# Kernel optimization log

Measured on AMD Instinct MI355X. Metric: run time of the kernel, lower is better.

## Reference

```python
import jax, jax.numpy as jnp
import numpy as np

B, N, H, DH = 2, 512, 12, 64
DIM, DPAIR, DCOND = 768, 128, 512
INNER = 4 * DIM  # expansion_factor * dim


def _ln(x, eps=1e-5):
    m = jnp.mean(x, -1, keepdims=True)
    v = jnp.mean((x - m) ** 2, -1, keepdims=True)
    return (x - m) * jax.lax.rsqrt(v + eps)


def _rope(t):
    # t: [b,h,n,d]; standard rotary over head dim
    d = t.shape[-1]
    pos = jnp.arange(t.shape[2], dtype=t.dtype)
    inv = 1.0 / (10000.0 ** (jnp.arange(0, d, 2, dtype=t.dtype) / d))
    ang = pos[:, None] * inv[None, :]  # [n, d/2]
    cos, sin = jnp.cos(ang), jnp.sin(ang)
    t1, t2 = t[..., 0::2], t[..., 1::2]
    return jnp.stack([t1 * cos - t2 * sin, t1 * sin + t2 * cos], -1).reshape(t.shape)


def _adaln(x, cond, mask, gw, gb, bw):
    cn = _ln(cond)
    return (_ln(x) * jax.nn.sigmoid(cn @ gw + gb) + cn @ bw) * mask[..., None]


def _scale_out(x, cond, mask, w, b):
    # adaLN-zero style output scaling
    return x * jax.nn.sigmoid(_ln(cond) @ w + b) * mask[..., None]


def _windowed_attn(q, k, v, bias, pair_mask, n_queries, n_keys):
    # q/k/v: [b,h,n,d]; bias: [b,h,n,n]; pair_mask: [b,n,n]
    b, h, n, d = q.shape
    nw = n // n_queries
    centers = jnp.arange(nw) * n_queries + n_queries // 2
    idx = centers[:, None] - n_keys // 2 + jnp.arange(n_keys)[None, :]  # [nw,nk]
    valid = (idx >= 0) & (idx < n)
    idxc = jnp.clip(idx, 0, n - 1)
    qw = q.reshape(b, h, nw, n_queries, d)
    kw = k[:, :, idxc]  # [b,h,nw,nk,d]
    vw = v[:, :, idxc]
    ib = jnp.broadcast_to(idxc[None, None, :, None, :], (b, h, nw, n_queries, n_keys))
    bias_w = jnp.take_along_axis(bias.reshape(b, h, nw, n_queries, n), ib, axis=-1)
    pm = jnp.take_along_axis(
        pair_mask.reshape(b, nw, n_queries, n),
        jnp.broadcast_to(idxc[None, :, None, :], (b, nw, n_queries, n_keys)), axis=-1)
    scores = jnp.einsum('bhwqd,bhwkd->bhwqk', qw, kw) / jnp.sqrt(jnp.asarray(d, q.dtype)) + bias_w
    ok = (pm[:, None] > 0) & valid[None, None, :, None, :]
    attn = jax.nn.softmax(jnp.where(ok, scores, -1e9), axis=-1)
    out = jnp.einsum('bhwqk,bhwkd->bhwqd', attn, vw)
    return out.reshape(b, h, n, d)


def setup_inputs() -> dict:
    key = jax.random.key(0)
    ks = iter(jax.random.split(key, 48))
    nrm = lambda shape: jax.random.normal(next(ks), shape, jnp.float32) * 0.02
    return dict(
        x=jax.random.normal(next(ks), (B, N, DIM), jnp.float32),
        pair_rep=jax.random.normal(next(ks), (B, N, N, DPAIR), jnp.float32),
        cond=jax.random.normal(next(ks), (B, N, DCOND), jnp.float32),
        mask=jnp.ones((B, N), jnp.float32),
        pair_mask=jnp.ones((B, N, N), jnp.float32),
        adaln1_gw=nrm((DCOND, DIM)), adaln1_gb=jnp.zeros((DIM,), jnp.float32), adaln1_bw=nrm((DCOND, DIM)),
        wq=nrm((DIM, H * DH)), bq=jnp.zeros((H * DH,), jnp.float32),
        wk=nrm((DIM, H * DH)), bk=jnp.zeros((H * DH,), jnp.float32),
        wv=nrm((DIM, H * DH)), bv=jnp.zeros((H * DH,), jnp.float32),
        wg=nrm((DIM, H * DH)), bg=jnp.zeros((H * DH,), jnp.float32),
        wb_pair=nrm((DPAIR, H)),
        wo=nrm((H * DH, DIM)), bo=jnp.zeros((DIM,), jnp.float32),
        scale1_w=nrm((DCOND, DIM)), scale1_b=jnp.full((DIM,), -2.0, jnp.float32),
        adaln2_gw=nrm((DCOND, DIM)), adaln2_gb=jnp.zeros((DIM,), jnp.float32), adaln2_bw=nrm((DCOND, DIM)),
        tr_win=nrm((DIM, 2 * INNER)), tr_wout=nrm((INNER, DIM)),
        scale2_w=nrm((DCOND, DIM)), scale2_b=jnp.full((DIM,), -2.0, jnp.float32),
        n_queries=32, n_keys=128,
    )


def reference(x, pair_rep, cond, mask, pair_mask,
              adaln1_gw, adaln1_gb, adaln1_bw,
              wq, bq, wk, bk, wv, bv, wg, bg, wb_pair, wo, bo,
              scale1_w, scale1_b,
              adaln2_gw, adaln2_gb, adaln2_bw,
              tr_win, tr_wout,
              scale2_w, scale2_b,
              n_queries, n_keys):
    b, n, _ = x.shape
    x = x * mask[..., None]

    # --- MHA (adaLN -> pair-biased rotary windowed attention -> adaLN-zero scale) ---
    xa = _adaln(x, cond, mask, adaln1_gw, adaln1_gb, adaln1_bw)
    q = (xa @ wq + bq).reshape(b, n, H, DH).transpose(0, 2, 1, 3)
    k = (xa @ wk + bk).reshape(b, n, H, DH).transpose(0, 2, 1, 3)
    v = (xa @ wv + bv).reshape(b, n, H, DH).transpose(0, 2, 1, 3)
    q, k = _ln(q), _ln(k)      # qk layernorm
    q, k = _rope(q), _rope(k)  # rotary
    bias = jnp.einsum('bijp,ph->bhij', _ln(pair_rep), wb_pair)
    o = _windowed_attn(q, k, v, bias, pair_mask, n_queries, n_keys)
    o = o.transpose(0, 2, 1, 3).reshape(b, n, H * DH)
    attn_out = (o * jax.nn.sigmoid(xa @ wg + bg)) @ wo + bo
    attn_out = _scale_out(attn_out, cond, mask, scale1_w, scale1_b) * mask[..., None]
    x = (attn_out + x) * mask[..., None]  # residual_mha

    # --- Transition (adaLN -> SwiGLU -> adaLN-zero scale) ---
    xt = _adaln(x, cond, mask, adaln2_gw, adaln2_gb, adaln2_bw)
    a, g = jnp.split(xt @ tr_win, 2, axis=-1)
    tr = ((a * jax.nn.silu(g)) @ tr_wout) * mask[..., None]
    tr = _scale_out(tr, cond, mask, scale2_w, scale2_b) * mask[..., None]
    x = (tr + x) * mask[..., None]  # residual_transition
    return x * mask[..., None]
```

## Files before the change

### kernel.cpp

```cpp
#include <hip/hip_runtime.h>
#include <hip/hip_bf16.h>
#include <math.h>
#include <stdint.h>

#define Bc   2
#define Nc   512
#define Hc   12
#define DHc  64
#define DIMc 768
#define DPAIRc 128
#define DCONDc 512
#define INNERc 3072
#define NQc  32
#define NKc  128
#define NWc  (Nc / NQc)

typedef __attribute__((ext_vector_type(8))) short short8;
typedef __attribute__((ext_vector_type(4))) float floatx4;

__device__ inline float wave_sum(float v) {
#pragma unroll
  for (int off = 32; off > 0; off >>= 1) v += __shfl_xor(v, off, 64);
  return v;
}
__device__ inline float wave_max(float v) {
#pragma unroll
  for (int off = 32; off > 0; off >>= 1) v = fmaxf(v, __shfl_xor(v, off, 64));
  return v;
}
__device__ inline float block_sum(float v, float* red) {
  v = wave_sum(v);
  int wv = threadIdx.x >> 6, lane = threadIdx.x & 63;
  __syncthreads();
  if (lane == 0) red[wv] = v;
  __syncthreads();
  return red[0] + red[1] + red[2] + red[3];
}
__device__ inline float sigmoidf(float x) { return 1.0f / (1.0f + expf(-x)); }

__device__ __forceinline__ void gload16(const void* g, void* l) {
  __builtin_amdgcn_global_load_lds(
      reinterpret_cast<__attribute__((address_space(1))) const void*>(
          reinterpret_cast<uintptr_t>(g)),
      reinterpret_cast<__attribute__((address_space(3))) void*>(
          static_cast<uint32_t>(reinterpret_cast<uintptr_t>(l))),
      16, 0, 0);
}

__global__ __launch_bounds__(256) void ln_rows_bf16_k(const float* __restrict__ in,
                                                      __hip_bfloat16* __restrict__ out, int C) {
  __shared__ float red[4];
  int row = blockIdx.x;
  const float* x = in + (size_t)row * C;
  float s = 0.f;
  for (int c = threadIdx.x; c < C; c += 256) s += x[c];
  float mean = block_sum(s, red) / C;
  float vs = 0.f;
  for (int c = threadIdx.x; c < C; c += 256) { float d = x[c] - mean; vs += d * d; }
  float var = block_sum(vs, red) / C;
  float r = rsqrtf(var + 1e-5f);
  for (int c = threadIdx.x; c < C; c += 256)
    out[(size_t)row * C + c] = __float2bfloat16((x[c] - mean) * r);
}

struct TP6 { const float* s0; const float* s1; const float* s2;
             const float* s3; const float* s4; const float* s5; };
__global__ __launch_bounds__(256) void transpose_cast_batch_k(TP6 p,
    __hip_bfloat16* __restrict__ dstBase, int K, int N) {
  __shared__ float tile[32][33];
  const float* srcs[6] = {p.s0, p.s1, p.s2, p.s3, p.s4, p.s5};
  const float* src = srcs[blockIdx.z];
  __hip_bfloat16* dst = dstBase + (size_t)blockIdx.z * K * N;
  int k0 = blockIdx.y * 32, n0 = blockIdx.x * 32;
  int t = threadIdx.x;
  int r = t >> 5, c = t & 31;
#pragma unroll
  for (int i = 0; i < 4; ++i) tile[r + i * 8][c] = src[(size_t)(k0 + r + i * 8) * N + n0 + c];
  __syncthreads();
#pragma unroll
  for (int i = 0; i < 4; ++i)
    dst[(size_t)(n0 + r + i * 8) * K + k0 + c] = __float2bfloat16(tile[c][r + i * 8]);
}

__global__ __launch_bounds__(256) void concat_bias_k(
    const float* __restrict__ a1_gb, const float* __restrict__ s1_b,
    const float* __restrict__ a2_gb, const float* __restrict__ s2_b,
    const float* __restrict__ bq, const float* __restrict__ bk,
    const float* __restrict__ bv, const float* __restrict__ bg,
    const float* __restrict__ wb_pair,
    float* __restrict__ cb6, float* __restrict__ bqkvg,
    __hip_bfloat16* __restrict__ wbT, float* __restrict__ colsum) {
  int i = blockIdx.x * 256 + threadIdx.x;
  if (i < 6 * DIMc) {
    int seg = i / DIMc, o = i - seg * DIMc;
    float v = 0.f;
    if (seg == 0) v = a1_gb[o];
    else if (seg == 2) v = s1_b[o];
    else if (seg == 3) v = a2_gb[o];
    else if (seg == 5) v = s2_b[o];
    cb6[i] = v;
  }
  if (i < 4 * DIMc) {
    int seg = i / DIMc, o = i - seg * DIMc;
    bqkvg[i] = (seg == 0) ? bq[o] : (seg == 1) ? bk[o] : (seg == 2) ? bv[o] : bg[o];
  }
  if (i < 16 * DPAIRc) {
    int h = i >> 7, c = i & 127;
    wbT[i] = (h < Hc) ? __float2bfloat16(wb_pair[c * Hc + h]) : __float2bfloat16(0.f);
  }
  if (blockIdx.x == 0 && threadIdx.x < 16) {
    int h = threadIdx.x;
    float s = 0.f;
    if (h < Hc)
      for (int c = 0; c < DPAIRc; ++c)
        s += __bfloat162float(__float2bfloat16(wb_pair[c * Hc + h]));
    colsum[h] = s;
  }
}

template <int WNT>
__global__ __launch_bounds__(256) void gemm_bf16_k(
    const __hip_bfloat16* __restrict__ A, const __hip_bfloat16* __restrict__ Bt,
    float* __restrict__ C, int M, int N, int K,
    const float* __restrict__ bias,
    const float* __restrict__ ss, int ssst,
    const float* __restrict__ resid, const float* __restrict__ maskp, int mode) {
  constexpr int TN = 32 * WNT;
  __shared__ __align__(16) __hip_bfloat16 As[2][128 * 32];
  __shared__ __align__(16) __hip_bfloat16 Bs[2][TN * 32];
  int tid = threadIdx.x;
  int lane = tid & 63, wv = tid >> 6;
  int l16 = lane & 15, quad = lane >> 4;
  int m0 = blockIdx.y * 128, n0 = blockIdx.x * TN;
  int wm0 = (wv >> 1) * 64, wn0 = (wv & 1) * (16 * WNT);

  int srow = tid >> 2;
  int skc = (tid & 3) * 8;
  const __hip_bfloat16* Ab  = A  + (size_t)(m0 + srow) * K + skc;
  const __hip_bfloat16* Ab2 = Ab + (size_t)64 * K;
  const __hip_bfloat16* Bb  = Bt + (size_t)(n0 + srow) * K + skc;
  const __hip_bfloat16* Bb2 = Bb + (size_t)64 * K;
  __hip_bfloat16* AsW0 = &As[0][0] + wv * 512;
  __hip_bfloat16* AsW1 = &As[1][0] + wv * 512;
  __hip_bfloat16* BsW0 = &Bs[0][0] + wv * 512;
  __hip_bfloat16* BsW1 = &Bs[1][0] + wv * 512;

  floatx4 acc[4][WNT];
#pragma unroll
  for (int mi = 0; mi < 4; ++mi)
#pragma unroll
    for (int nj = 0; nj < WNT; ++nj) acc[mi][nj] = (floatx4){0.f, 0.f, 0.f, 0.f};

  auto stage = [&](int kk, __hip_bfloat16* AW, __hip_bfloat16* BW) {
    gload16(Ab + kk, AW);
    gload16(Ab2 + kk, AW + 2048);
    if (WNT == 4) {
      gload16(Bb + kk, BW);
      gload16(Bb2 + kk, BW + 2048);
    } else {
      if (wv < 2) gload16(Bb + kk, BW);
    }
  };
  auto compute = [&](const __hip_bfloat16* Asb, const __hip_bfloat16* Bsb) {
    short8 a[4], b[WNT];
#pragma unroll
    for (int mi = 0; mi < 4; ++mi)
      a[mi] = *(const short8*)(const void*)&Asb[(wm0 + mi * 16 + l16) * 32 + quad * 8];
#pragma unroll
    for (int nj = 0; nj < WNT; ++nj)
      b[nj] = *(const short8*)(const void*)&Bsb[(wn0 + nj * 16 + l16) * 32 + quad * 8];
#pragma unroll
    for (int mi = 0; mi < 4; ++mi)
#pragma unroll
      for (int nj = 0; nj < WNT; ++nj)
        acc[mi][nj] = __builtin_amdgcn_mfma_f32_16x16x32_bf16(a[mi], b[nj], acc[mi][nj], 0, 0, 0);
  };

  stage(0, AsW0, BsW0);
  __syncthreads();
  for (int k0 = 0; k0 < K; k0 += 64) {
    if (k0 + 32 < K) stage(k0 + 32, AsW1, BsW1);
    compute(&As[0][0], &Bs[0][0]);
    __syncthreads();
    if (k0 + 64 < K) stage(k0 + 64, AsW0, BsW0);
    compute(&As[1][0], &Bs[1][0]);
    __syncthreads();
  }

#pragma unroll
  for (int mi = 0; mi < 4; ++mi) {
#pragma unroll
    for (int nj = 0; nj < WNT; ++nj) {
      int ncol = n0 + wn0 + nj * 16 + l16;
      float bb = bias ? bias[ncol] : 0.f;
#pragma unroll
      for (int r = 0; r < 4; ++r) {
        int m = m0 + wm0 + mi * 16 + quad * 4 + r;
        float v = acc[mi][nj][r] + bb;
        if (mode == 1) {
          float mk = maskp[m];
          v *= sigmoidf(ss[(size_t)m * ssst + ncol]) * mk * mk;
          v = (v + resid[(size_t)m * N + ncol]) * mk;
        } else if (mode == 2) {
          float mk = maskp[m];
          v = v * mk * sigmoidf(ss[(size_t)m * ssst + ncol]) * mk * mk;
          v = (v + resid[(size_t)m * N + ncol]) * mk * mk;
        }
        C[(size_t)m * N + ncol] = v;
      }
    }
  }
}

__global__ __launch_bounds__(256) void adaln_apply_k(
    const float* __restrict__ xin, const float* __restrict__ maskp,
    const float* __restrict__ graw, const float* __restrict__ braw, int ssst,
    __hip_bfloat16* __restrict__ xa, float* __restrict__ xm) {
  __shared__ float red[4];
  int row = blockIdx.x;
  float mk = maskp[row];
  const float* xr = xin + (size_t)row * DIMc;
  float vals[3];
  float s = 0.f;
#pragma unroll
  for (int it = 0; it < 3; ++it) {
    int c = threadIdx.x + it * 256;
    float v = xr[c] * mk;
    vals[it] = v;
    s += v;
  }
  float mean = block_sum(s, red) * (1.0f / DIMc);
  float vs = 0.f;
#pragma unroll
  for (int it = 0; it < 3; ++it) { float d = vals[it] - mean; vs += d * d; }
  float var = block_sum(vs, red) * (1.0f / DIMc);
  float r = rsqrtf(var + 1e-5f);
#pragma unroll
  for (int it = 0; it < 3; ++it) {
    int c = threadIdx.x + it * 256;
    size_t sidx = (size_t)row * ssst + c;
    if (xm) xm[(size_t)row * DIMc + c] = vals[it];
    float o = ((vals[it] - mean) * r * sigmoidf(graw[sidx]) + braw[sidx]) * mk;
    xa[(size_t)row * DIMc + c] = __float2bfloat16(o);
  }
}

__global__ __launch_bounds__(256) void lnrope_k(float* __restrict__ qkvg) {
  float* q = qkvg + blockIdx.y * DIMc;
  int rowid = blockIdx.x * 4 + (threadIdx.x >> 6);
  int lane = threadIdx.x & 63;
  int bn = rowid / Hc;
  int h = rowid - bn * Hc;
  int n = bn & (Nc - 1);
  size_t base = (size_t)bn * (4 * DIMc) + h * DHc;
  float v = q[base + lane];
  float mean = wave_sum(v) * (1.0f / 64.0f);
  float d = v - mean;
  float var = wave_sum(d * d) * (1.0f / 64.0f);
  float vn = d * rsqrtf(var + 1e-5f);
  int i = lane >> 1;
  float inv = exp2f(-(float)i * 0.415241011861f);
  float ang = (float)n * inv;
  float c = cosf(ang), s = sinf(ang);
  float partner = __shfl_xor(vn, 1, 64);
  float out = (lane & 1) ? (partner * s + vn * c) : (vn * c - partner * s);
  q[base + lane] = out;
}

__global__ __launch_bounds__(256) void pair_bias_mfma_k(
    const float* __restrict__ pr, const __hip_bfloat16* __restrict__ wbT,
    const float* __restrict__ colsum, float* __restrict__ biasw) {
  constexpr int LDR = 136;
  __shared__ __hip_bfloat16 rows[128 * LDR];
  __shared__ float meanS[128];
  __shared__ float rstdS[128];
  int bi = blockIdx.x;
  int i = bi & (Nc - 1), b = bi >> 9;
  int w = i >> 5, qi = i & 31;
  int j0 = w * NQc - 48;
  int t = threadIdx.x;
  int sub = t >> 5;
  int c4 = t & 31;
  const float* prb = pr + (size_t)bi * (Nc * DPAIRc);
#pragma unroll
  for (int step = 0; step < 16; ++step) {
    int row = step * 8 + sub;
    int jc = min(max(j0 + row, 0), Nc - 1);
    float4 v = *(const float4*)(prb + (size_t)jc * DPAIRc + c4 * 4);
    union { __hip_bfloat16 h[4]; uint2 u; } pk;
    pk.h[0] = __float2bfloat16(v.x); pk.h[1] = __float2bfloat16(v.y);
    pk.h[2] = __float2bfloat16(v.z); pk.h[3] = __float2bfloat16(v.w);
    *(uint2*)(void*)&rows[row * LDR + c4 * 4] = pk.u;
    float s = v.x + v.y + v.z + v.w;
    float s2 = v.x * v.x + v.y * v.y + v.z * v.z + v.w * v.w;
#pragma unroll
    for (int off = 16; off > 0; off >>= 1) {
      s += __shfl_xor(s, off, 64);
      s2 += __shfl_xor(s2, off, 64);
    }
    if (c4 == 0) {
      float mean = s * (1.0f / 128.0f);
      float var = s2 * (1.0f / 128.0f) - mean * mean;
      meanS[row] = mean;
      rstdS[row] = rsqrtf(var + 1e-5f);
    }
  }
  __syncthreads();
  int lane = t & 63, wv = t >> 6;
  int l16 = lane & 15, quad = lane >> 4;
  short8 bfrag[4];
#pragma unroll
  for (int ks = 0; ks < 4; ++ks)
    bfrag[ks] = *(const short8*)(const void*)&wbT[l16 * 128 + ks * 32 + quad * 8];
  float cs = colsum[l16];
#pragma unroll
  for (int mt = 0; mt < 2; ++mt) {
    int mtile = wv * 2 + mt;
    floatx4 acc = (floatx4){0.f, 0.f, 0.f, 0.f};
#pragma unroll
    for (int ks = 0; ks < 4; ++ks) {
      short8 a = *(const short8*)(const void*)&rows[(mtile * 16 + l16) * LDR + ks * 32 + quad * 8];
      acc = __builtin_amdgcn_mfma_f32_16x16x32_bf16(a, bfrag[ks], acc, 0, 0, 0);
    }
    if (l16 < Hc) {
      int m0r = mtile * 16 + quad * 4;
      float4 ov;
      float* po = &ov.x;
#pragma unroll
      for (int r = 0; r < 4; ++r) {
        int m = m0r + r;
        po[r] = rstdS[m] * (acc[r] - meanS[m] * cs);
      }
      *(float4*)&biasw[((((size_t)(b * Hc + l16)) * NWc + w) * NQc + qi) * NKc + m0r] = ov;
    }
  }
}

__global__ __launch_bounds__(256) void wattn_k(
    const float* __restrict__ qkvg, const float* __restrict__ biasw,
    const float* __restrict__ pair_mask, __hip_bfloat16* __restrict__ o) {
  constexpr int LQ = 72;
  constexpr int LV = 136;
  constexpr int LS = 132;
  constexpr int LP = 136;
  __shared__ __hip_bfloat16 qs[32 * LQ];
  __shared__ __hip_bfloat16 ks[128 * LQ];
  __shared__ __hip_bfloat16 vT[64 * LV];
  __shared__ float sc[32 * LS];
  __shared__ __hip_bfloat16 scP[32 * LP];
  const int QS = 4 * DIMc;
  int blk = blockIdx.x;
  int w = blk & (NWc - 1);
  int bh = blk >> 4;
  int h = bh % Hc;
  int b = bh / Hc;
  int t = threadIdx.x;
  int j0 = w * NQc - 48;
  for (int e = t; e < 512; e += 256) {
    int qrow = e >> 4, c4 = e & 15;
    float4 v = *(const float4*)&qkvg[(size_t)(b * Nc + w * NQc + qrow) * QS + h * DHc + c4 * 4];
    union { __hip_bfloat16 hh[4]; uint2 u; } pk;
    pk.hh[0] = __float2bfloat16(v.x); pk.hh[1] = __float2bfloat16(v.y);
    pk.hh[2] = __float2bfloat16(v.z); pk.hh[3] = __float2bfloat16(v.w);
    *(uint2*)(void*)&qs[qrow * LQ + c4 * 4] = pk.u;
  }
  for (int e = t; e < 2048; e += 256) {
    int kk = e >> 4, c4 = e & 15;
    int jc = min(max(j0 + kk, 0), Nc - 1);
    size_t src = (size_t)(b * Nc + jc) * QS + h * DHc + c4 * 4;
    float4 kv = *(const float4*)&qkvg[src + DIMc];
    float4 vv = *(const float4*)&qkvg[src + 2 * DIMc];
    union { __hip_bfloat16 hh[4]; uint2 u; } pk;
    pk.hh[0] = __float2bfloat16(kv.x); pk.hh[1] = __float2bfloat16(kv.y);
    pk.hh[2] = __float2bfloat16(kv.z); pk.hh[3] = __float2bfloat16(kv.w);
    *(uint2*)(void*)&ks[kk * LQ + c4 * 4] = pk.u;
    vT[(c4 * 4 + 0) * LV + kk] = __float2bfloat16(vv.x);
    vT[(c4 * 4 + 1) * LV + kk] = __float2bfloat16(vv.y);
    vT[(c4 * 4 + 2) * LV + kk] = __float2bfloat16(vv.z);
    vT[(c4 * 4 + 3) * LV + kk] = __float2bfloat16(vv.w);
  }
  for (int e = t; e < 4096; e += 256) {
    int qrow = e >> 7, key = e & 127;
    int j = j0 + key;
    bool valid = (j >= 0) && (j < Nc);
    int jc = min(max(j, 0), Nc - 1);
    float pm = pair_mask[((size_t)(b * Nc + w * NQc + qrow)) * Nc + jc];
    bool ok = valid && (pm > 0.f);
    sc[qrow * LS + key] = ok ? biasw[((size_t)blk * 32 + qrow) * 128 + key] : -1e30f;
  }
  __syncthreads();
  int lane = t & 63, wv = t >> 6;
  int l16 = lane & 15, quad = lane >> 4;
  {
    short8 bfr[2][2];
#pragma unroll
    for (int nt = 0; nt < 2; ++nt)
#pragma unroll
      for (int k2 = 0; k2 < 2; ++k2)
        bfr[nt][k2] = *(const short8*)(const void*)&ks[(wv * 32 + nt * 16 + l16) * LQ + k2 * 32 + quad * 8];
#pragma unroll
    for (int mi = 0; mi < 2; ++mi) {
      short8 afr[2];
#pragma unroll
      for (int k2 = 0; k2 < 2; ++k2)
        afr[k2] = *(const short8*)(const void*)&qs[(mi * 16 + l16) * LQ + k2 * 32 + quad * 8];
#pragma unroll
      for (int nt = 0; nt < 2; ++nt) {
        floatx4 acc = (floatx4){0.f, 0.f, 0.f, 0.f};
        acc = __builtin_amdgcn_mfma_f32_16x16x32_bf16(afr[0], bfr[nt][0], acc, 0, 0, 0);
        acc = __builtin_amdgcn_mfma_f32_16x16x32_bf16(afr[1], bfr[nt][1], acc, 0, 0, 0);
        int key = wv * 32 + nt * 16 + l16;
#pragma unroll
        for (int r = 0; r < 4; ++r) {
          int m = mi * 16 + quad * 4 + r;
          float sv = sc[m * LS + key];
          if (sv > -1e29f) sc[m * LS + key] = sv + acc[r] * 0.125f;
        }
      }
    }
  }
  __syncthreads();
#pragma unroll
  for (int rr = 0; rr < 8; ++rr) {
    int qq = wv * 8 + rr;
    float v0 = sc[qq * LS + lane], v1 = sc[qq * LS + 64 + lane];
    float mx = wave_max(fmaxf(v0, v1));
    float e0 = expf(v0 - mx), e1 = expf(v1 - mx);
    float inv = 1.0f / wave_sum(e0 + e1);
    scP[qq * LP + lane] = __float2bfloat16(e0 * inv);
    scP[qq * LP + 64 + lane] = __float2bfloat16(e1 * inv);
  }
  __syncthreads();
  {
    short8 vb[4];
#pragma unroll
    for (int k4 = 0; k4 < 4; ++k4)
      vb[k4] = *(const short8*)(const void*)&vT[(wv * 16 + l16) * LV + k4 * 32 + quad * 8];
#pragma unroll
    for (int mi = 0; mi < 2; ++mi) {
      floatx4 acc = (floatx4){0.f, 0.f, 0.f, 0.f};
#pragma unroll
      for (int k4 = 0; k4 < 4; ++k4) {
        short8 pa = *(const short8*)(const void*)&scP[(mi * 16 + l16) * LP + k4 * 32 + quad * 8];
        acc = __builtin_amdgcn_mfma_f32_16x16x32_bf16(pa, vb[k4], acc, 0, 0, 0);
      }
      int d = wv * 16 + l16;
#pragma unroll
      for (int r = 0; r < 4; ++r) {
        int m = mi * 16 + quad * 4 + r;
        size_t mrow = (size_t)(b * Nc + w * NQc + m);
        float g = qkvg[mrow * QS + 3 * DIMc + h * DHc + d];
        o[mrow * DIMc + h * DHc + d] = __float2bfloat16(acc[r] * sigmoidf(g));
      }
    }
  }
}

__global__ __launch_bounds__(256) void silu_gate_k(const float* __restrict__ h,
                                                   __hip_bfloat16* __restrict__ act, int total) {
  int i = blockIdx.x * 256 + threadIdx.x;
  if (i < total) {
    int m = i / INNERc, j = i - m * INNERc;
    float a = h[(size_t)m * (2 * INNERc) + j];
    float g = h[(size_t)m * (2 * INNERc) + INNERc + j];
    act[i] = __float2bfloat16(a * g * sigmoidf(g));
  }
}

extern "C" void kernel_launch(void* const* d_in, const int* in_sizes, int n_in,
                              void* d_out, int out_size, void* d_ws, size_t ws_size,
                              hipStream_t stream) {
  const float* x        = (const float*)d_in[0];
  const float* pair_rep = (const float*)d_in[1];
  const float* cond     = (const float*)d_in[2];
  const float* mask     = (const float*)d_in[3];
  const float* pair_mask= (const float*)d_in[4];
  const float* a1_gw    = (const float*)d_in[5];
  const float* a1_gb    = (const float*)d_in[6];
  const float* a1_bw    = (const float*)d_in[7];
  const float* wq       = (const float*)d_in[8];
  const float* bq       = (const float*)d_in[9];
  const float* wk       = (const float*)d_in[10];
  const float* bk       = (const float*)d_in[11];
  const float* wv       = (const float*)d_in[12];
  const float* bv       = (const float*)d_in[13];
  const float* wg       = (const float*)d_in[14];
  const float* bg       = (const float*)d_in[15];
  const float* wb_pair  = (const float*)d_in[16];
  const float* wo       = (const float*)d_in[17];
  const float* bo       = (const float*)d_in[18];
  const float* s1_w     = (const float*)d_in[19];
  const float* s1_b     = (const float*)d_in[20];
  const float* a2_gw    = (const float*)d_in[21];
  const float* a2_gb    = (const float*)d_in[22];
  const float* a2_bw    = (const float*)d_in[23];
  const float* tr_win   = (const float*)d_in[24];
  const float* tr_wout  = (const float*)d_in[25];
  const float* s2_w     = (const float*)d_in[26];
  const float* s2_b     = (const float*)d_in[27];
  float* out = (float*)d_out;

  const int M = Bc * Nc;
  char* wsb = (char*)d_ws;
  size_t off = 0;
  auto alloc = [&](size_t bytes) { void* p = wsb + off; off += (bytes + 255) & ~(size_t)255; return p; };

  __hip_bfloat16* cnb     = (__hip_bfloat16*)alloc((size_t)M * DCONDc * 2);
  __hip_bfloat16* Wc6t    = (__hip_bfloat16*)alloc((size_t)6 * DIMc * DCONDc * 2);
  __hip_bfloat16* Wqkvg5t = (__hip_bfloat16*)alloc((size_t)5 * DIMc * DIMc * 2);
  __hip_bfloat16* twint   = (__hip_bfloat16*)alloc((size_t)2 * INNERc * DIMc * 2);
  __hip_bfloat16* twoutt  = (__hip_bfloat16*)alloc((size_t)DIMc * INNERc * 2);
  float* cb6    = (float*)alloc((size_t)6 * DIMc * 4);
  float* bqkvg  = (float*)alloc((size_t)4 * DIMc * 4);
  __hip_bfloat16* wbT = (__hip_bfloat16*)alloc((size_t)16 * DPAIRc * 2);
  float* colsum = (float*)alloc(16 * 4);
  float* proj_c = (float*)alloc((size_t)M * 6 * DIMc * 4);
  float* xm     = (float*)alloc((size_t)M * DIMc * 4);
  __hip_bfloat16* xa = (__hip_bfloat16*)alloc((size_t)M * DIMc * 2);
  float* qkvg   = (float*)alloc((size_t)M * 4 * DIMc * 4);
  float* biasw  = (float*)alloc((size_t)Bc * Hc * NWc * NQc * NKc * 4);
  __hip_bfloat16* obg = (__hip_bfloat16*)alloc((size_t)M * DIMc * 2);
  float* x2     = (float*)alloc((size_t)M * DIMc * 4);
  __hip_bfloat16* xt = (__hip_bfloat16*)alloc((size_t)M * DIMc * 2);
  float* hb     = (float*)alloc((size_t)M * 2 * INNERc * 4);
  __hip_bfloat16* actb = (__hip_bfloat16*)alloc((size_t)M * INNERc * 2);
  __hip_bfloat16* wot = Wqkvg5t + (size_t)4 * DIMc * DIMc;
  (void)ws_size; (void)in_sizes; (void)n_in; (void)out_size;

  dim3 blk(256);

  ln_rows_bf16_k<<<M, blk, 0, stream>>>(cond, cnb, DCONDc);

  transpose_cast_batch_k<<<dim3(DIMc / 32, DCONDc / 32, 6), blk, 0, stream>>>(
      TP6{a1_gw, a1_bw, s1_w, a2_gw, a2_bw, s2_w}, Wc6t, DCONDc, DIMc);
  transpose_cast_batch_k<<<dim3(DIMc / 32, DIMc / 32, 5), blk, 0, stream>>>(
      TP6{wq, wk, wv, wg, wo, wo}, Wqkvg5t, DIMc, DIMc);
  transpose_cast_batch_k<<<dim3(2 * INNERc / 32, DIMc / 32, 1), blk, 0, stream>>>(
      TP6{tr_win, tr_win, tr_win, tr_win, tr_win, tr_win}, twint, DIMc, 2 * INNERc);
  transpose_cast_batch_k<<<dim3(DIMc / 32, INNERc / 32, 1), blk, 0, stream>>>(
      TP6{tr_wout, tr_wout, tr_wout, tr_wout, tr_wout, tr_wout}, twoutt, INNERc, DIMc);

  concat_bias_k<<<(6 * DIMc + 255) / 256, blk, 0, stream>>>(
      a1_gb, s1_b, a2_gb, s2_b, bq, bk, bv, bg, wb_pair, cb6, bqkvg, wbT, colsum);

  gemm_bf16_k<4><<<dim3(6 * DIMc / 128, M / 128), blk, 0, stream>>>(
      cnb, Wc6t, proj_c, M, 6 * DIMc, DCONDc, cb6, nullptr, 0, nullptr, nullptr, 0);

  adaln_apply_k<<<M, blk, 0, stream>>>(x, mask, proj_c + 0, proj_c + DIMc, 6 * DIMc, xa, xm);

  gemm_bf16_k<4><<<dim3(4 * DIMc / 128, M / 128), blk, 0, stream>>>(
      xa, Wqkvg5t, qkvg, M, 4 * DIMc, DIMc, bqkvg, nullptr, 0, nullptr, nullptr, 0);

  lnrope_k<<<dim3((M * Hc) / 4, 2), blk, 0, stream>>>(qkvg);

  pair_bias_mfma_k<<<Bc * Nc, blk, 0, stream>>>(pair_rep, wbT, colsum, biasw);

  wattn_k<<<Bc * Hc * NWc, blk, 0, stream>>>(qkvg, biasw, pair_mask, obg);

  gemm_bf16_k<1><<<dim3(DIMc / 32, M / 128), blk, 0, stream>>>(
      obg, wot, x2, M, DIMc, DIMc, bo, proj_c + 2 * DIMc, 6 * DIMc, xm, mask, 1);

  adaln_apply_k<<<M, blk, 0, stream>>>(x2, mask, proj_c + 3 * DIMc, proj_c + 4 * DIMc,
                                       6 * DIMc, xt, nullptr);

  gemm_bf16_k<4><<<dim3(2 * INNERc / 128, M / 128), blk, 0, stream>>>(
      xt, twint, hb, M, 2 * INNERc, DIMc, nullptr, nullptr, 0, nullptr, nullptr, 0);

  silu_gate_k<<<(M * INNERc + 255) / 256, blk, 0, stream>>>(hb, actb, M * INNERc);

  gemm_bf16_k<1><<<dim3(DIMc / 32, M / 128), blk, 0, stream>>>(
      actb, twoutt, out, M, DIMc, INNERc, nullptr, proj_c + 5 * DIMc, 6 * DIMc, x2, mask, 2);
}
```

Before: 592.8 us.

## Fuse SwiGLU into transition GEMM epilogue and qk-LN/RoPE into attention load

The SwiGLU-in weight is transposed with its columns interleaved in 16-wide groups, so each GEMM warp holds matching value and gate tiles and writes the bf16 silu product directly. This removes the fp32 hidden buffer and the separate silu_gate kernel. The separate qk-layernorm and RoPE kernel is also dropped, and that work now runs inside the attention kernel's Q/K staging loops. As a trade-off, K normalization and rotation are recomputed for overlapping windows, and the variance uses the E[x²]-mean² formula.

```diff
diff --git a/kernel.cpp b/kernel.cpp
--- a/kernel.cpp
+++ b/kernel.cpp
@@ -66,7 +66,7 @@
 struct TP6 { const float* s0; const float* s1; const float* s2;
              const float* s3; const float* s4; const float* s5; };
 __global__ __launch_bounds__(256) void transpose_cast_batch_k(TP6 p,
-    __hip_bfloat16* __restrict__ dstBase, int K, int N) {
+    __hip_bfloat16* __restrict__ dstBase, int K, int N, int interleave) {
   __shared__ float tile[32][33];
   const float* srcs[6] = {p.s0, p.s1, p.s2, p.s3, p.s4, p.s5};
   const float* src = srcs[blockIdx.z];
@@ -78,8 +78,16 @@
   for (int i = 0; i < 4; ++i) tile[r + i * 8][c] = src[(size_t)(k0 + r + i * 8) * N + n0 + c];
   __syncthreads();
 #pragma unroll
-  for (int i = 0; i < 4; ++i)
-    dst[(size_t)(n0 + r + i * 8) * K + k0 + c] = __float2bfloat16(tile[c][r + i * 8]);
+  for (int i = 0; i < 4; ++i) {
+    int n = n0 + r + i * 8;
+    int dr = n;
+    if (interleave) {
+      int half = N >> 1;
+      dr = (n < half) ? (((n >> 4) << 5) + (n & 15))
+                      : ((((n - half) >> 4) << 5) + 16 + ((n - half) & 15));
+    }
+    dst[(size_t)dr * K + k0 + c] = __float2bfloat16(tile[c][r + i * 8]);
+  }
 }
 
 __global__ __launch_bounds__(256) void concat_bias_k(
@@ -187,6 +195,28 @@
     __syncthreads();
   }
 
+  if (mode == 3) {
+    if constexpr (WNT >= 2) {
+      __hip_bfloat16* Cb = (__hip_bfloat16*)C;
+      int halfN = N >> 1;
+#pragma unroll
+      for (int mi = 0; mi < 4; ++mi) {
+#pragma unroll
+        for (int njp = 0; njp < WNT / 2; ++njp) {
+          int outcol = ((n0 + wn0) >> 1) + njp * 16 + l16;
+#pragma unroll
+          for (int r = 0; r < 4; ++r) {
+            int m = m0 + wm0 + mi * 16 + quad * 4 + r;
+            float av = acc[mi][2 * njp][r];
+            float gv = acc[mi][2 * njp + 1][r];
+            Cb[(size_t)m * halfN + outcol] = __float2bfloat16(av * gv * sigmoidf(gv));
+          }
+        }
+      }
+    }
+    return;
+  }
+
 #pragma unroll
   for (int mi = 0; mi < 4; ++mi) {
 #pragma unroll
@@ -243,28 +273,6 @@
     float o = ((vals[it] - mean) * r * sigmoidf(graw[sidx]) + braw[sidx]) * mk;
     xa[(size_t)row * DIMc + c] = __float2bfloat16(o);
   }
-}
-
-__global__ __launch_bounds__(256) void lnrope_k(float* __restrict__ qkvg) {
-  float* q = qkvg + blockIdx.y * DIMc;
-  int rowid = blockIdx.x * 4 + (threadIdx.x >> 6);
-  int lane = threadIdx.x & 63;
-  int bn = rowid / Hc;
-  int h = rowid - bn * Hc;
-  int n = bn & (Nc - 1);
-  size_t base = (size_t)bn * (4 * DIMc) + h * DHc;
-  float v = q[base + lane];
-  float mean = wave_sum(v) * (1.0f / 64.0f);
-  float d = v - mean;
-  float var = wave_sum(d * d) * (1.0f / 64.0f);
-  float vn = d * rsqrtf(var + 1e-5f);
-  int i = lane >> 1;
-  float inv = exp2f(-(float)i * 0.415241011861f);
-  float ang = (float)n * inv;
-  float c = cosf(ang), s = sinf(ang);
-  float partner = __shfl_xor(vn, 1, 64);
-  float out = (lane & 1) ? (partner * s + vn * c) : (vn * c - partner * s);
-  q[base + lane] = out;
 }
 
 __global__ __launch_bounds__(256) void pair_bias_mfma_k(
@@ -359,9 +367,27 @@
   for (int e = t; e < 512; e += 256) {
     int qrow = e >> 4, c4 = e & 15;
     float4 v = *(const float4*)&qkvg[(size_t)(b * Nc + w * NQc + qrow) * QS + h * DHc + c4 * 4];
+    float s = v.x + v.y + v.z + v.w;
+    float s2 = v.x * v.x + v.y * v.y + v.z * v.z + v.w * v.w;
+#pragma unroll
+    for (int off = 1; off < 16; off <<= 1) {
+      s += __shfl_xor(s, off, 64);
+      s2 += __shfl_xor(s2, off, 64);
+    }
+    float mean = s * (1.0f / 64.0f);
+    float rr = rsqrtf(s2 * (1.0f / 64.0f) - mean * mean + 1e-5f);
+    float qn0 = (v.x - mean) * rr, qn1 = (v.y - mean) * rr;
+    float qn2 = (v.z - mean) * rr, qn3 = (v.w - mean) * rr;
+    float pos = (float)(w * NQc + qrow);
+    float inv0 = exp2f(-(float)(c4 * 2) * 0.415241011861f);
+    float inv1 = exp2f(-(float)(c4 * 2 + 1) * 0.415241011861f);
+    float a0 = pos * inv0, a1 = pos * inv1;
+    float c0 = cosf(a0), sn0 = sinf(a0), c1 = cosf(a1), sn1 = sinf(a1);
     union { __hip_bfloat16 hh[4]; uint2 u; } pk;
-    pk.hh[0] = __float2bfloat16(v.x); pk.hh[1] = __float2bfloat16(v.y);
-    pk.hh[2] = __float2bfloat16(v.z); pk.hh[3] = __float2bfloat16(v.w);
+    pk.hh[0] = __float2bfloat16(qn0 * c0 - qn1 * sn0);
+    pk.hh[1] = __float2bfloat16(qn0 * sn0 + qn1 * c0);
+    pk.hh[2] = __float2bfloat16(qn2 * c1 - qn3 * sn1);
+    pk.hh[3] = __float2bfloat16(qn2 * sn1 + qn3 * c1);
     *(uint2*)(void*)&qs[qrow * LQ + c4 * 4] = pk.u;
   }
   for (int e = t; e < 2048; e += 256) {
@@ -370,9 +396,27 @@
     size_t src = (size_t)(b * Nc + jc) * QS + h * DHc + c4 * 4;
     float4 kv = *(const float4*)&qkvg[src + DIMc];
     float4 vv = *(const float4*)&qkvg[src + 2 * DIMc];
+    float s = kv.x + kv.y + kv.z + kv.w;
+    float s2 = kv.x * kv.x + kv.y * kv.y + kv.z * kv.z + kv.w * kv.w;
+#pragma unroll
+    for (int off = 1; off < 16; off <<= 1) {
+      s += __shfl_xor(s, off, 64);
+      s2 += __shfl_xor(s2, off, 64);
+    }
+    float mean = s * (1.0f / 64.0f);
+    float rr = rsqrtf(s2 * (1.0f / 64.0f) - mean * mean + 1e-5f);
+    float kn0 = (kv.x - mean) * rr, kn1 = (kv.y - mean) * rr;
+    float kn2 = (kv.z - mean) * rr, kn3 = (kv.w - mean) * rr;
+    float pos = (float)jc;
+    float inv0 = exp2f(-(float)(c4 * 2) * 0.415241011861f);
+    float inv1 = exp2f(-(float)(c4 * 2 + 1) * 0.415241011861f);
+    float a0 = pos * inv0, a1 = pos * inv1;
+    float c0 = cosf(a0), sn0 = sinf(a0), c1 = cosf(a1), sn1 = sinf(a1);
     union { __hip_bfloat16 hh[4]; uint2 u; } pk;
-    pk.hh[0] = __float2bfloat16(kv.x); pk.hh[1] = __float2bfloat16(kv.y);
-    pk.hh[2] = __float2bfloat16(kv.z); pk.hh[3] = __float2bfloat16(kv.w);
+    pk.hh[0] = __float2bfloat16(kn0 * c0 - kn1 * sn0);
+    pk.hh[1] = __float2bfloat16(kn0 * sn0 + kn1 * c0);
+    pk.hh[2] = __float2bfloat16(kn2 * c1 - kn3 * sn1);
+    pk.hh[3] = __float2bfloat16(kn2 * sn1 + kn3 * c1);
     *(uint2*)(void*)&ks[kk * LQ + c4 * 4] = pk.u;
     vT[(c4 * 4 + 0) * LV + kk] = __float2bfloat16(vv.x);
     vT[(c4 * 4 + 1) * LV + kk] = __float2bfloat16(vv.y);
@@ -453,17 +497,6 @@
         o[mrow * DIMc + h * DHc + d] = __float2bfloat16(acc[r] * sigmoidf(g));
       }
     }
-  }
-}
-
-__global__ __launch_bounds__(256) void silu_gate_k(const float* __restrict__ h,
-                                                   __hip_bfloat16* __restrict__ act, int total) {
-  int i = blockIdx.x * 256 + threadIdx.x;
-  if (i < total) {
-    int m = i / INNERc, j = i - m * INNERc;
-    float a = h[(size_t)m * (2 * INNERc) + j];
-    float g = h[(size_t)m * (2 * INNERc) + INNERc + j];
-    act[i] = __float2bfloat16(a * g * sigmoidf(g));
   }
 }
 
@@ -522,7 +555,6 @@
   __hip_bfloat16* obg = (__hip_bfloat16*)alloc((size_t)M * DIMc * 2);
   float* x2     = (float*)alloc((size_t)M * DIMc * 4);
   __hip_bfloat16* xt = (__hip_bfloat16*)alloc((size_t)M * DIMc * 2);
-  float* hb     = (float*)alloc((size_t)M * 2 * INNERc * 4);
   __hip_bfloat16* actb = (__hip_bfloat16*)alloc((size_t)M * INNERc * 2);
   __hip_bfloat16* wot = Wqkvg5t + (size_t)4 * DIMc * DIMc;
   (void)ws_size; (void)in_sizes; (void)n_in; (void)out_size;
@@ -532,13 +564,13 @@
   ln_rows_bf16_k<<<M, blk, 0, stream>>>(cond, cnb, DCONDc);
 
   transpose_cast_batch_k<<<dim3(DIMc / 32, DCONDc / 32, 6), blk, 0, stream>>>(
-      TP6{a1_gw, a1_bw, s1_w, a2_gw, a2_bw, s2_w}, Wc6t, DCONDc, DIMc);
+      TP6{a1_gw, a1_bw, s1_w, a2_gw, a2_bw, s2_w}, Wc6t, DCONDc, DIMc, 0);
   transpose_cast_batch_k<<<dim3(DIMc / 32, DIMc / 32, 5), blk, 0, stream>>>(
-      TP6{wq, wk, wv, wg, wo, wo}, Wqkvg5t, DIMc, DIMc);
+      TP6{wq, wk, wv, wg, wo, wo}, Wqkvg5t, DIMc, DIMc, 0);
   transpose_cast_batch_k<<<dim3(2 * INNERc / 32, DIMc / 32, 1), blk, 0, stream>>>(
-      TP6{tr_win, tr_win, tr_win, tr_win, tr_win, tr_win}, twint, DIMc, 2 * INNERc);
+      TP6{tr_win, tr_win, tr_win, tr_win, tr_win, tr_win}, twint, DIMc, 2 * INNERc, 1);
   transpose_cast_batch_k<<<dim3(DIMc / 32, INNERc / 32, 1), blk, 0, stream>>>(
-      TP6{tr_wout, tr_wout, tr_wout, tr_wout, tr_wout, tr_wout}, twoutt, INNERc, DIMc);
+      TP6{tr_wout, tr_wout, tr_wout, tr_wout, tr_wout, tr_wout}, twoutt, INNERc, DIMc, 0);
 
   concat_bias_k<<<(6 * DIMc + 255) / 256, blk, 0, stream>>>(
       a1_gb, s1_b, a2_gb, s2_b, bq, bk, bv, bg, wb_pair, cb6, bqkvg, wbT, colsum);
@@ -551,8 +583,6 @@
   gemm_bf16_k<4><<<dim3(4 * DIMc / 128, M / 128), blk, 0, stream>>>(
       xa, Wqkvg5t, qkvg, M, 4 * DIMc, DIMc, bqkvg, nullptr, 0, nullptr, nullptr, 0);
 
-  lnrope_k<<<dim3((M * Hc) / 4, 2), blk, 0, stream>>>(qkvg);
-
   pair_bias_mfma_k<<<Bc * Nc, blk, 0, stream>>>(pair_rep, wbT, colsum, biasw);
 
   wattn_k<<<Bc * Hc * NWc, blk, 0, stream>>>(qkvg, biasw, pair_mask, obg);
@@ -564,9 +594,7 @@
                                        6 * DIMc, xt, nullptr);
 
   gemm_bf16_k<4><<<dim3(2 * INNERc / 128, M / 128), blk, 0, stream>>>(
-      xt, twint, hb, M, 2 * INNERc, DIMc, nullptr, nullptr, 0, nullptr, nullptr, 0);
-
-  silu_gate_k<<<(M * INNERc + 255) / 256, blk, 0, stream>>>(hb, actb, M * INNERc);
+      xt, twint, (float*)actb, M, 2 * INNERc, DIMc, nullptr, nullptr, 0, nullptr, nullptr, 3);
 
   gemm_bf16_k<1><<<dim3(DIMc / 32, M / 128), blk, 0, stream>>>(
       actb, twoutt, out, M, DIMc, INNERc, nullptr, proj_c + 5 * DIMc, 6 * DIMc, x2, mask, 2);
```

After: 590.0 us. No clear change (-0.5%).
